# Performance work log

Hardware: AMD Instinct MI355X
Metric: run time of the kernel (lower is better)

Reference implementation:

```python
import jax, jax.numpy as jnp
import numpy as np

D_MODEL = 256
D_INNER = 512      # expand=2 * d_model
D_STATE = 16
D_CONV = 4
DT_RANK = 16       # ceil(d_model/16)
BT, N = 16, 1024


def setup_inputs() -> dict:
    key = jax.random.key(0)
    ks = jax.random.split(key, 8)
    def w(k, shape, scale=0.02):
        return jax.random.normal(k, shape, dtype=jnp.float32) * scale
    token = jax.random.normal(ks[0], (BT, N, D_MODEL), dtype=jnp.float32)
    in_proj_w = w(ks[1], (2 * D_INNER, D_MODEL))
    conv_w = w(ks[2], (D_INNER, D_CONV), 0.1)          # depthwise conv taps
    conv_b = jnp.zeros((D_INNER,), jnp.float32)
    x_proj_w = w(ks[3], (DT_RANK + 2 * D_STATE, D_INNER))
    dt_proj_w = w(ks[4], (D_INNER, DT_RANK), 0.1)
    # softplus^{-1}(0.01): standard Mamba dt bias init scale
    dt_proj_b = jnp.log(jnp.expm1(jnp.full((D_INNER,), 0.01, jnp.float32)))
    # S4D-real init: A_log = log(1..d_state) per channel
    A_log = jnp.log(jnp.tile(jnp.arange(1, D_STATE + 1, dtype=jnp.float32), (D_INNER, 1)))
    D_skip = jnp.ones((D_INNER,), jnp.float32)
    out_proj_w = w(ks[5], (D_MODEL, D_INNER))
    return dict(token=token, in_proj_w=in_proj_w, conv_w=conv_w, conv_b=conv_b,
                x_proj_w=x_proj_w, dt_proj_w=dt_proj_w, dt_proj_b=dt_proj_b,
                A_log=A_log, D_skip=D_skip, out_proj_w=out_proj_w)


def _mamba_fwd(token, in_proj_w, conv_w, conv_b, x_proj_w, dt_proj_w, dt_proj_b,
               A_log, D_skip, out_proj_w):
    B, L, _ = token.shape
    # input projection -> gate z and conv branch x
    xz = jnp.einsum('blc,ec->ble', token, in_proj_w)        # (B,L,2*Di)
    x, z = jnp.split(xz, 2, axis=-1)                        # (B,L,Di) each
    # depthwise causal conv1d, kernel D_CONV, left padding D_CONV-1
    xp = jnp.pad(x, ((0, 0), (D_CONV - 1, 0), (0, 0)))
    x_conv = conv_b + sum(xp[:, k:k + L, :] * conv_w[:, k] for k in range(D_CONV))
    x = jax.nn.silu(x_conv)
    # data-dependent dt, B, C
    dbc = jnp.einsum('bld,ed->ble', x, x_proj_w)            # (B,L,dt_rank+2*Ns)
    dt, Bm, Cm = jnp.split(dbc, [DT_RANK, DT_RANK + D_STATE], axis=-1)
    delta = jax.nn.softplus(jnp.einsum('blr,dr->bld', dt, dt_proj_w) + dt_proj_b)
    A = -jnp.exp(A_log)                                     # (Di,Ns), all negative
    dA = jnp.exp(delta[..., None] * A)                      # (B,L,Di,Ns)
    dBu = delta[..., None] * Bm[:, :, None, :] * x[..., None]  # (B,L,Di,Ns)
    # selective scan over sequence: h_t = dA_t * h_{t-1} + dBu_t ; y_t = <h_t, C_t>
    def step(h, inp):
        dA_t, dBu_t, C_t = inp                              # (B,Di,Ns),(B,Di,Ns),(B,Ns)
        h = dA_t * h + dBu_t
        y = jnp.einsum('bdn,bn->bd', h, C_t)
        return h, y
    h0 = jnp.zeros((B, D_INNER, D_STATE), token.dtype)
    xs = (dA.transpose(1, 0, 2, 3), dBu.transpose(1, 0, 2, 3), Cm.transpose(1, 0, 2))
    _, ys = jax.lax.scan(step, h0, xs)                      # (L,B,Di)
    y = ys.transpose(1, 0, 2) + x * D_skip
    y = y * jax.nn.silu(z)
    return jnp.einsum('bld,cd->blc', y, out_proj_w)         # (B,L,d_model)


def reference(token, in_proj_w, conv_w, conv_b, x_proj_w, dt_proj_w, dt_proj_b,
              A_log, D_skip, out_proj_w):
    return _mamba_fwd(token, in_proj_w, conv_w, conv_b, x_proj_w, dt_proj_w,
                      dt_proj_b, A_log, D_skip, out_proj_w)
```

## Files before the change

kernel.cpp:

```cpp
#include <hip/hip_runtime.h>
#include <cstddef>

static constexpr int kDModel = 256;
static constexpr int kDInner = 512;
static constexpr int kDState = 16;
static constexpr int kDtRank = 16;
static constexpr int kB = 16;
static constexpr int kL = 1024;
static constexpr int kTok = kB * kL;
static constexpr int kDbcW = kDtRank + 2 * kDState;
static constexpr int kT = 64;
static constexpr int kG = kL / kT;

typedef __attribute__((ext_vector_type(8))) short short8;
typedef __attribute__((ext_vector_type(4))) float f32x4;

__device__ __forceinline__ float siluf(float x) {
  return x / (1.0f + __expf(-x));
}

__device__ __forceinline__ void split2(float a, float b, unsigned& h, unsigned& l) {
  const unsigned ua = __float_as_uint(a), ub = __float_as_uint(b);
  const unsigned ha = ua & 0xffff0000u, hb = ub & 0xffff0000u;
  h = (ha >> 16) | hb;
  const float la = a - __uint_as_float(ha);
  const float lb = b - __uint_as_float(hb);
  l = (__float_as_uint(la) >> 16) | (__float_as_uint(lb) & 0xffff0000u);
}

__global__ __launch_bounds__(256) void split_k(
    const float* __restrict__ src, unsigned short* __restrict__ H,
    unsigned short* __restrict__ L, int n4)
{
  const int i = (int)(blockIdx.x * 256 + threadIdx.x);
  if (i >= n4) return;
  const float4 v = ((const float4*)src)[i];
  unsigned h0, l0, h1, l1;
  split2(v.x, v.y, h0, l0);
  split2(v.z, v.w, h1, l1);
  ((uint2*)H)[i] = make_uint2(h0, h1);
  ((uint2*)L)[i] = make_uint2(l0, l1);
}

__device__ __forceinline__ void gload16(const unsigned short* g, unsigned short* l) {
  __builtin_amdgcn_global_load_lds(
      (const __attribute__((address_space(1))) unsigned int*)g,
      (__attribute__((address_space(3))) unsigned int*)l, 16, 0, 0);
}

template <int EPI>
__global__ __launch_bounds__(256) void gemm_bt_mfma(
    const unsigned short* __restrict__ Ahg, const unsigned short* __restrict__ Alg, int lda,
    const unsigned short* __restrict__ Bhg, const unsigned short* __restrict__ Blg, int ldb,
    float* __restrict__ C, int ldc, int K,
    float* __restrict__ out2)
{
  __shared__ __align__(16) unsigned short lds[12288];
  unsigned short* Ah = lds;
  unsigned short* Al = lds + 4096;
  unsigned short* Bh = lds + 8192;
  unsigned short* Bl = lds + 10240;

  const int tid = (int)threadIdx.x;
  const int m0 = blockIdx.x * 128;
  const int n0 = blockIdx.y * 64;
  const int lane = tid & 63;
  const int w = tid >> 6, wm = w >> 1, wn = w & 1;
  const int fr = lane & 15;
  const int j = lane >> 4;

  const int srow = lane >> 2;
  const int sslot = lane & 3;

  f32x4 acc[4][2];
#pragma unroll
  for (int i = 0; i < 4; ++i)
#pragma unroll
    for (int jj = 0; jj < 2; ++jj) acc[i][jj] = (f32x4){0.f, 0.f, 0.f, 0.f};

  const int r1 = 16 * w + srow;
  const int r2 = r1 + 64;
  const int s1 = (sslot ^ ((r1 >> 1) & 3)) * 8;
  const int s2 = (sslot ^ ((r2 >> 1) & 3)) * 8;
  const unsigned short* A1h = Ahg + (size_t)(m0 + r1) * lda + s1;
  const unsigned short* A2h = Ahg + (size_t)(m0 + r2) * lda + s2;
  const unsigned short* A1l = Alg + (size_t)(m0 + r1) * lda + s1;
  const unsigned short* A2l = Alg + (size_t)(m0 + r2) * lda + s2;
  const unsigned short* B1h = Bhg + (size_t)(n0 + r1) * ldb + s1;
  const unsigned short* B1l = Blg + (size_t)(n0 + r1) * ldb + s1;
  unsigned short* dA1 = Ah + 512 * w;
  unsigned short* dA2 = Ah + 512 * (w + 4);
  unsigned short* dL1 = Al + 512 * w;
  unsigned short* dL2 = Al + 512 * (w + 4);
  unsigned short* dB1 = Bh + 512 * w;
  unsigned short* dB2 = Bl + 512 * w;

  for (int k0 = 0; k0 < K; k0 += 32) {
    __syncthreads();
    gload16(A1h + k0, dA1);
    gload16(A2h + k0, dA2);
    gload16(A1l + k0, dL1);
    gload16(A2l + k0, dL2);
    gload16(B1h + k0, dB1);
    gload16(B1l + k0, dB2);
    __syncthreads();

    short8 ah[4], al[4], bh[2], bl[2];
#pragma unroll
    for (int mi = 0; mi < 4; ++mi) {
      const int R = wm * 64 + mi * 16 + fr;
      const int off = R * 32 + ((j ^ ((R >> 1) & 3)) * 8);
      ah[mi] = *(const short8*)&Ah[off];
      al[mi] = *(const short8*)&Al[off];
    }
#pragma unroll
    for (int ni = 0; ni < 2; ++ni) {
      const int R = wn * 32 + ni * 16 + fr;
      const int off = R * 32 + ((j ^ ((R >> 1) & 3)) * 8);
      bh[ni] = *(const short8*)&Bh[off];
      bl[ni] = *(const short8*)&Bl[off];
    }
#pragma unroll
    for (int mi = 0; mi < 4; ++mi)
#pragma unroll
      for (int ni = 0; ni < 2; ++ni) {
        acc[mi][ni] = __builtin_amdgcn_mfma_f32_16x16x32_bf16(ah[mi], bh[ni], acc[mi][ni], 0, 0, 0);
        acc[mi][ni] = __builtin_amdgcn_mfma_f32_16x16x32_bf16(ah[mi], bl[ni], acc[mi][ni], 0, 0, 0);
        acc[mi][ni] = __builtin_amdgcn_mfma_f32_16x16x32_bf16(al[mi], bh[ni], acc[mi][ni], 0, 0, 0);
      }
  }

  float* Cb;
  int nbase, ldout;
  if (EPI == 1) {
    Cb = (n0 < kDInner) ? C : out2;
    nbase = (n0 & (kDInner - 1)) + wn * 32 + fr;
    ldout = kDInner;
  } else {
    Cb = C;
    nbase = n0 + wn * 32 + fr;
    ldout = ldc;
  }
#pragma unroll
  for (int mi = 0; mi < 4; ++mi) {
    const int mrow = m0 + wm * 64 + mi * 16 + (lane >> 4) * 4;
#pragma unroll
    for (int ni = 0; ni < 2; ++ni)
#pragma unroll
      for (int r = 0; r < 4; ++r)
        Cb[(size_t)(mrow + r) * ldout + nbase + ni * 16] = acc[mi][ni][r];
  }
}

template <int EPI>
__global__ __launch_bounds__(256) void gemm_bt_f32(
    const float* __restrict__ A, int lda,
    const float* __restrict__ B, int ldb,
    float* __restrict__ C, int ldc,
    int N, int K,
    float* __restrict__ out2,
    const float* __restrict__ bias)
{
  constexpr int BM = 64, BN = 64, BK = 16;
  __shared__ float As[BK][BM];
  __shared__ float Bs[BK][BN];
  const int m0 = blockIdx.x * BM;
  const int n0 = blockIdx.y * BN;
  const int tid = (int)threadIdx.x;
  const int tx = tid & 15;
  const int ty = tid >> 4;
  const int lr = tid >> 2;
  const int lk = (tid & 3) * 4;

  float acc[4][4] = {};

  for (int k0 = 0; k0 < K; k0 += BK) {
    const float4 a4 = *(const float4*)(A + (size_t)(m0 + lr) * lda + k0 + lk);
    float4 b4 = make_float4(0.f, 0.f, 0.f, 0.f);
    if (n0 + lr < N)
      b4 = *(const float4*)(B + (size_t)(n0 + lr) * ldb + k0 + lk);
    __syncthreads();
    As[lk + 0][lr] = a4.x; As[lk + 1][lr] = a4.y;
    As[lk + 2][lr] = a4.z; As[lk + 3][lr] = a4.w;
    Bs[lk + 0][lr] = b4.x; Bs[lk + 1][lr] = b4.y;
    Bs[lk + 2][lr] = b4.z; Bs[lk + 3][lr] = b4.w;
    __syncthreads();
#pragma unroll
    for (int kk = 0; kk < BK; ++kk) {
      const float4 av = *(const float4*)&As[kk][ty * 4];
      const float4 bv = *(const float4*)&Bs[kk][tx * 4];
      const float a[4] = {av.x, av.y, av.z, av.w};
      const float b[4] = {bv.x, bv.y, bv.z, bv.w};
#pragma unroll
      for (int i = 0; i < 4; ++i)
#pragma unroll
        for (int j = 0; j < 4; ++j)
          acc[i][j] = fmaf(a[i], b[j], acc[i][j]);
    }
  }

#pragma unroll
  for (int i = 0; i < 4; ++i) {
    const int m = m0 + ty * 4 + i;
#pragma unroll
    for (int j = 0; j < 4; ++j) {
      const int n = n0 + tx * 4 + j;
      float v = acc[i][j];
      if (EPI == 0) {
        if (n < N) C[(size_t)m * ldc + n] = v;
      } else {
        v += bias[n];
        v = fmaxf(v, 0.f) + __logf(1.f + __expf(-fabsf(v)));
        if (n < N) C[(size_t)m * ldc + n] = v;
      }
    }
  }
}

__global__ __launch_bounds__(256) void conv_silu_k(
    const float* __restrict__ x, const float* __restrict__ cw,
    const float* __restrict__ cb, float* __restrict__ xc)
{
  const int id = (int)(blockIdx.x * 256 + threadIdx.x);
  const int dq = (id & 127) * 4;
  const int t  = id >> 7;
  const int l  = t & (kL - 1);

  float w[4][4];
#pragma unroll
  for (int j = 0; j < 4; ++j) {
    const float4 wt = *(const float4*)(cw + (size_t)(dq + j) * 4);
    w[j][0] = wt.x; w[j][1] = wt.y; w[j][2] = wt.z; w[j][3] = wt.w;
  }
  float r[4] = {cb[dq + 0], cb[dq + 1], cb[dq + 2], cb[dq + 3]};
#pragma unroll
  for (int k = 0; k < 4; ++k) {
    const int ll = l + k - 3;
    if (ll >= 0) {
      const float4 xv = *(const float4*)(x + (size_t)(t + k - 3) * kDInner + dq);
      r[0] = fmaf(xv.x, w[0][k], r[0]);
      r[1] = fmaf(xv.y, w[1][k], r[1]);
      r[2] = fmaf(xv.z, w[2][k], r[2]);
      r[3] = fmaf(xv.w, w[3][k], r[3]);
    }
  }
  *(float4*)(xc + (size_t)t * kDInner + dq) =
      make_float4(siluf(r[0]), siluf(r[1]), siluf(r[2]), siluf(r[3]));
}

__global__ __launch_bounds__(256) void scan_part1(
    const float* __restrict__ delta, const float* __restrict__ xc,
    const float* __restrict__ dbc,  const float* __restrict__ A_log,
    float* __restrict__ Pbuf, float* __restrict__ hloc)
{
  const int tid = (int)(blockIdx.x * 256 + threadIdx.x);
  const int lane = tid & 63;
  const int gw = __builtin_amdgcn_readfirstlane(tid >> 6);
  const int dg = gw & 7;
  const int c  = (gw >> 3) & (kG - 1);
  const int b  = gw >> 7;
  const int d  = dg * 64 + lane;
  const int t0 = b * kL + c * kT;

  float A2[kDState], h[kDState];
#pragma unroll
  for (int n = 0; n < kDState; ++n) {
    A2[n] = -__expf(A_log[d * kDState + n]) * 1.44269504088896f;
    h[n] = 0.f;
  }
  const float* dp = delta + (size_t)t0 * kDInner + d;
  const float* xp = xc + (size_t)t0 * kDInner + d;
  float sd = 0.f;
#pragma unroll 2
  for (int l = 0; l < kT; ++l) {
    const float dl = dp[(size_t)l * kDInner];
    const float xv = xp[(size_t)l * kDInner];
    const float* bp = dbc + (size_t)(t0 + l) * kDbcW + kDtRank;
    const float s = dl * xv;
    sd += dl;
#pragma unroll
    for (int n = 0; n < kDState; ++n) {
      const float dA = __builtin_amdgcn_exp2f(dl * A2[n]);
      h[n] = fmaf(dA, h[n], s * bp[n]);
    }
  }
  const size_t o0 = (size_t)((b * kG + c) * kDState) * kDInner + d;
#pragma unroll
  for (int n = 0; n < kDState; ++n) {
    Pbuf[o0 + (size_t)n * kDInner] = __builtin_amdgcn_exp2f(A2[n] * sd);
    hloc[o0 + (size_t)n * kDInner] = h[n];
  }
}

__global__ __launch_bounds__(256) void scan_part2(
    const float* __restrict__ Pbuf, const float* __restrict__ hloc,
    float* __restrict__ hin)
{
  const int t = (int)(blockIdx.x * 256 + threadIdx.x);
  const int d = t & (kDInner - 1);
  const int n = (t >> 9) & (kDState - 1);
  const int b = t >> 13;
  float carry = 0.f;
#pragma unroll
  for (int c = 0; c < kG; ++c) {
    const size_t idx = (size_t)((b * kG + c) * kDState + n) * kDInner + d;
    hin[idx] = carry;
    carry = fmaf(Pbuf[idx], carry, hloc[idx]);
  }
}

__global__ __launch_bounds__(256) void scan_part3(
    const float* __restrict__ delta, const float* __restrict__ xc,
    const float* __restrict__ dbc,  const float* __restrict__ z,
    const float* __restrict__ A_log, const float* __restrict__ D_skip,
    const float* __restrict__ hin,
    unsigned short* __restrict__ yh, unsigned short* __restrict__ yl)
{
  const int tid = (int)(blockIdx.x * 256 + threadIdx.x);
  const int lane = tid & 63;
  const int gw = __builtin_amdgcn_readfirstlane(tid >> 6);
  const int dg = gw & 7;
  const int c  = (gw >> 3) & (kG - 1);
  const int b  = gw >> 7;
  const int d  = dg * 64 + lane;
  const int t0 = b * kL + c * kT;

  const size_t o0 = (size_t)((b * kG + c) * kDState) * kDInner + d;
  float A2[kDState], h[kDState];
#pragma unroll
  for (int n = 0; n < kDState; ++n) {
    A2[n] = -__expf(A_log[d * kDState + n]) * 1.44269504088896f;
    h[n] = hin[o0 + (size_t)n * kDInner];
  }
  const float Dv = D_skip[d];
  const float* dp = delta + (size_t)t0 * kDInner + d;
  const float* xp = xc + (size_t)t0 * kDInner + d;
  const float* zp = z + (size_t)t0 * kDInner + d;
  unsigned short* yhp = yh + (size_t)t0 * kDInner + d;
  unsigned short* ylp = yl + (size_t)t0 * kDInner + d;
#pragma unroll 2
  for (int l = 0; l < kT; ++l) {
    const float dl = dp[(size_t)l * kDInner];
    const float xv = xp[(size_t)l * kDInner];
    const float zv = zp[(size_t)l * kDInner];
    const float* bp = dbc + (size_t)(t0 + l) * kDbcW + kDtRank;
    const float s = dl * xv;
    float yv = 0.f;
#pragma unroll
    for (int n = 0; n < kDState; ++n) {
      const float dA = __builtin_amdgcn_exp2f(dl * A2[n]);
      h[n] = fmaf(dA, h[n], s * bp[n]);
      yv = fmaf(h[n], bp[kDState + n], yv);
    }
    yv = fmaf(xv, Dv, yv);
    yv *= zv / (1.f + __expf(-zv));
    const unsigned u = __float_as_uint(yv);
    const unsigned hi = u & 0xffff0000u;
    yhp[(size_t)l * kDInner] = (unsigned short)(u >> 16);
    ylp[(size_t)l * kDInner] =
        (unsigned short)(__float_as_uint(yv - __uint_as_float(hi)) >> 16);
  }
}

extern "C" void kernel_launch(void* const* d_in, const int* in_sizes, int n_in,
                              void* d_out, int out_size, void* d_ws, size_t ws_size,
                              hipStream_t stream) {
  (void)in_sizes; (void)n_in; (void)out_size; (void)ws_size;
  const float* token     = (const float*)d_in[0];
  const float* in_proj_w = (const float*)d_in[1];
  const float* conv_w    = (const float*)d_in[2];
  const float* conv_b    = (const float*)d_in[3];
  const float* x_proj_w  = (const float*)d_in[4];
  const float* dt_proj_w = (const float*)d_in[5];
  const float* dt_proj_b = (const float*)d_in[6];
  const float* A_log     = (const float*)d_in[7];
  const float* D_skip    = (const float*)d_in[8];
  const float* out_proj_w= (const float*)d_in[9];
  float* out = (float*)d_out;

  float* ws = (float*)d_ws;
  float* xbuf  = ws;
  float* zbuf  = xbuf + (size_t)kTok * kDInner;
  float* xcbuf = zbuf + (size_t)kTok * kDInner;
  float* dbc   = xcbuf + (size_t)kTok * kDInner;
  float* ybuf  = dbc + (size_t)kTok * kDbcW;
  float* hin   = ybuf + (size_t)kTok * kDInner;
  float* delta = xbuf;

  unsigned short* tokH = (unsigned short*)ybuf;
  unsigned short* tokL = tokH + (size_t)kTok * kDModel;
  float* Pbuf = ybuf;
  float* hloc = ybuf + (size_t)kB * kG * kDState * kDInner;
  unsigned short* yh = (unsigned short*)ybuf;
  unsigned short* yl = yh + (size_t)kTok * kDInner;
  unsigned short* ipH = (unsigned short*)hin;
  unsigned short* ipL = ipH + (size_t)2 * kDInner * kDModel;
  unsigned short* opH = (unsigned short*)(hin + (size_t)kB * kDInner * kG * kDState);
  unsigned short* opL = opH + (size_t)kDModel * kDInner;

  split_k<<<(kTok * kDModel / 4) / 256, 256, 0, stream>>>(token, tokH, tokL,
                                                          kTok * kDModel / 4);
  split_k<<<(2 * kDInner * kDModel / 4) / 256, 256, 0, stream>>>(
      in_proj_w, ipH, ipL, 2 * kDInner * kDModel / 4);
  split_k<<<(kDModel * kDInner / 4) / 256, 256, 0, stream>>>(
      out_proj_w, opH, opL, kDModel * kDInner / 4);

  {
    dim3 g(kTok / 128, (2 * kDInner) / 64);
    gemm_bt_mfma<1><<<g, 256, 0, stream>>>(tokH, tokL, kDModel, ipH, ipL, kDModel,
                                           xbuf, kDInner, kDModel, zbuf);
  }
  conv_silu_k<<<(kTok * (kDInner / 4)) / 256, 256, 0, stream>>>(xbuf, conv_w, conv_b, xcbuf);
  {
    dim3 g(kTok / 64, 1);
    gemm_bt_f32<0><<<g, 256, 0, stream>>>(xcbuf, kDInner, x_proj_w, kDInner,
                                          dbc, kDbcW, kDbcW, kDInner,
                                          nullptr, nullptr);
  }
  {
    dim3 g(kTok / 64, kDInner / 64);
    gemm_bt_f32<2><<<g, 256, 0, stream>>>(dbc, kDbcW, dt_proj_w, kDtRank,
                                          delta, kDInner, kDInner, kDtRank,
                                          nullptr, dt_proj_b);
  }
  scan_part1<<<(kB * kG * 8) / 4, 256, 0, stream>>>(delta, xcbuf, dbc, A_log,
                                                    Pbuf, hloc);
  scan_part2<<<(kB * kDInner * kDState) / 256, 256, 0, stream>>>(Pbuf, hloc, hin);
  scan_part3<<<(kB * kG * 8) / 4, 256, 0, stream>>>(delta, xcbuf, dbc, zbuf,
                                                    A_log, D_skip, hin, yh, yl);
  {
    dim3 g(kTok / 128, kDModel / 64);
    gemm_bt_mfma<0><<<g, 256, 0, stream>>>(yh, yl, kDInner, opH, opL, kDInner,
                                           out, kDModel, kDInner, nullptr);
  }
}
```

Measured before the change: 282.4 us.

## Fuse dt projection into scan kernels and double-buffer MFMA GEMM LDS loads

Removes the separate dt_proj GEMM+softplus kernel. Both scan passes now recompute delta per token and channel from the dbc row using per-thread dt_proj weights, which saves writing and reading the 32 MB delta buffer twice. The MFMA GEMM also gets a two-stage LDS double buffer, so the next K tile's global-to-LDS loads are issued before computing on the current one, with explicit vmcnt waits. The trade-off is extra FMAs and transcendentals recomputed in both scan passes, plus double the LDS footprint, which may reduce occupancy.

```diff
diff --git a/kernel.cpp b/kernel.cpp
--- a/kernel.cpp
+++ b/kernel.cpp
@@ -55,11 +55,7 @@
     float* __restrict__ C, int ldc, int K,
     float* __restrict__ out2)
 {
-  __shared__ __align__(16) unsigned short lds[12288];
-  unsigned short* Ah = lds;
-  unsigned short* Al = lds + 4096;
-  unsigned short* Bh = lds + 8192;
-  unsigned short* Bl = lds + 10240;
+  __shared__ __align__(16) unsigned short lds[24576];
 
   const int tid = (int)threadIdx.x;
   const int m0 = blockIdx.x * 128;
@@ -88,37 +84,44 @@
   const unsigned short* A2l = Alg + (size_t)(m0 + r2) * lda + s2;
   const unsigned short* B1h = Bhg + (size_t)(n0 + r1) * ldb + s1;
   const unsigned short* B1l = Blg + (size_t)(n0 + r1) * ldb + s1;
-  unsigned short* dA1 = Ah + 512 * w;
-  unsigned short* dA2 = Ah + 512 * (w + 4);
-  unsigned short* dL1 = Al + 512 * w;
-  unsigned short* dL2 = Al + 512 * (w + 4);
-  unsigned short* dB1 = Bh + 512 * w;
-  unsigned short* dB2 = Bl + 512 * w;
-
-  for (int k0 = 0; k0 < K; k0 += 32) {
-    __syncthreads();
-    gload16(A1h + k0, dA1);
-    gload16(A2h + k0, dA2);
-    gload16(A1l + k0, dL1);
-    gload16(A2l + k0, dL2);
-    gload16(B1h + k0, dB1);
-    gload16(B1l + k0, dB2);
-    __syncthreads();
+
+  auto STAGE = [&](unsigned short* buf, int k0) {
+    gload16(A1h + k0, buf + 512 * w);
+    gload16(A2h + k0, buf + 512 * (w + 4));
+    gload16(A1l + k0, buf + 4096 + 512 * w);
+    gload16(A2l + k0, buf + 4096 + 512 * (w + 4));
+    gload16(B1h + k0, buf + 8192 + 512 * w);
+    gload16(B1l + k0, buf + 10240 + 512 * w);
+  };
+
+  const int nt = K >> 5;
+  unsigned short* cur = lds;
+  unsigned short* nxt = lds + 12288;
+
+  STAGE(cur, 0);
+  for (int it = 0; it < nt; ++it) {
+    if (it + 1 < nt) {
+      STAGE(nxt, (it + 1) << 5);
+      asm volatile("s_waitcnt vmcnt(6)" ::: "memory");
+    } else {
+      asm volatile("s_waitcnt vmcnt(0)" ::: "memory");
+    }
+    __builtin_amdgcn_s_barrier();
 
     short8 ah[4], al[4], bh[2], bl[2];
 #pragma unroll
     for (int mi = 0; mi < 4; ++mi) {
       const int R = wm * 64 + mi * 16 + fr;
       const int off = R * 32 + ((j ^ ((R >> 1) & 3)) * 8);
-      ah[mi] = *(const short8*)&Ah[off];
-      al[mi] = *(const short8*)&Al[off];
+      ah[mi] = *(const short8*)&cur[off];
+      al[mi] = *(const short8*)&cur[4096 + off];
     }
 #pragma unroll
     for (int ni = 0; ni < 2; ++ni) {
       const int R = wn * 32 + ni * 16 + fr;
       const int off = R * 32 + ((j ^ ((R >> 1) & 3)) * 8);
-      bh[ni] = *(const short8*)&Bh[off];
-      bl[ni] = *(const short8*)&Bl[off];
+      bh[ni] = *(const short8*)&cur[8192 + off];
+      bl[ni] = *(const short8*)&cur[10240 + off];
     }
 #pragma unroll
     for (int mi = 0; mi < 4; ++mi)
@@ -128,6 +131,8 @@
         acc[mi][ni] = __builtin_amdgcn_mfma_f32_16x16x32_bf16(ah[mi], bl[ni], acc[mi][ni], 0, 0, 0);
         acc[mi][ni] = __builtin_amdgcn_mfma_f32_16x16x32_bf16(al[mi], bh[ni], acc[mi][ni], 0, 0, 0);
       }
+    __builtin_amdgcn_s_barrier();
+    unsigned short* t = cur; cur = nxt; nxt = t;
   }
 
   float* Cb;
@@ -152,14 +157,11 @@
   }
 }
 
-template <int EPI>
 __global__ __launch_bounds__(256) void gemm_bt_f32(
     const float* __restrict__ A, int lda,
     const float* __restrict__ B, int ldb,
     float* __restrict__ C, int ldc,
-    int N, int K,
-    float* __restrict__ out2,
-    const float* __restrict__ bias)
+    int N, int K)
 {
   constexpr int BM = 64, BN = 64, BK = 16;
   __shared__ float As[BK][BM];
@@ -205,14 +207,7 @@
 #pragma unroll
     for (int j = 0; j < 4; ++j) {
       const int n = n0 + tx * 4 + j;
-      float v = acc[i][j];
-      if (EPI == 0) {
-        if (n < N) C[(size_t)m * ldc + n] = v;
-      } else {
-        v += bias[n];
-        v = fmaxf(v, 0.f) + __logf(1.f + __expf(-fabsf(v)));
-        if (n < N) C[(size_t)m * ldc + n] = v;
-      }
+      if (n < N) C[(size_t)m * ldc + n] = acc[i][j];
     }
   }
 }
@@ -248,9 +243,18 @@
       make_float4(siluf(r[0]), siluf(r[1]), siluf(r[2]), siluf(r[3]));
 }
 
+__device__ __forceinline__ float delta_of(const float* __restrict__ row,
+                                          const float* __restrict__ W, float bias) {
+  float a = bias;
+#pragma unroll
+  for (int r = 0; r < kDtRank; ++r) a = fmaf(row[r], W[r], a);
+  return fmaxf(a, 0.f) + __logf(1.f + __expf(-fabsf(a)));
+}
+
 __global__ __launch_bounds__(256) void scan_part1(
-    const float* __restrict__ delta, const float* __restrict__ xc,
-    const float* __restrict__ dbc,  const float* __restrict__ A_log,
+    const float* __restrict__ xc, const float* __restrict__ dbc,
+    const float* __restrict__ A_log,
+    const float* __restrict__ dtW, const float* __restrict__ dtB,
     float* __restrict__ Pbuf, float* __restrict__ hloc)
 {
   const int tid = (int)(blockIdx.x * 256 + threadIdx.x);
@@ -262,26 +266,29 @@
   const int d  = dg * 64 + lane;
   const int t0 = b * kL + c * kT;
 
-  float A2[kDState], h[kDState];
+  float A2[kDState], h[kDState], W[kDtRank];
 #pragma unroll
   for (int n = 0; n < kDState; ++n) {
     A2[n] = -__expf(A_log[d * kDState + n]) * 1.44269504088896f;
     h[n] = 0.f;
   }
-  const float* dp = delta + (size_t)t0 * kDInner + d;
+#pragma unroll
+  for (int r = 0; r < kDtRank; ++r) W[r] = dtW[d * kDtRank + r];
+  const float bias = dtB[d];
+
   const float* xp = xc + (size_t)t0 * kDInner + d;
   float sd = 0.f;
 #pragma unroll 2
   for (int l = 0; l < kT; ++l) {
-    const float dl = dp[(size_t)l * kDInner];
     const float xv = xp[(size_t)l * kDInner];
-    const float* bp = dbc + (size_t)(t0 + l) * kDbcW + kDtRank;
+    const float* row = dbc + (size_t)(t0 + l) * kDbcW;
+    const float dl = delta_of(row, W, bias);
     const float s = dl * xv;
     sd += dl;
 #pragma unroll
     for (int n = 0; n < kDState; ++n) {
       const float dA = __builtin_amdgcn_exp2f(dl * A2[n]);
-      h[n] = fmaf(dA, h[n], s * bp[n]);
+      h[n] = fmaf(dA, h[n], s * row[kDtRank + n]);
     }
   }
   const size_t o0 = (size_t)((b * kG + c) * kDState) * kDInner + d;
@@ -310,9 +317,10 @@
 }
 
 __global__ __launch_bounds__(256) void scan_part3(
-    const float* __restrict__ delta, const float* __restrict__ xc,
-    const float* __restrict__ dbc,  const float* __restrict__ z,
-    const float* __restrict__ A_log, const float* __restrict__ D_skip,
+    const float* __restrict__ xc, const float* __restrict__ dbc,
+    const float* __restrict__ z,  const float* __restrict__ A_log,
+    const float* __restrict__ D_skip,
+    const float* __restrict__ dtW, const float* __restrict__ dtB,
     const float* __restrict__ hin,
     unsigned short* __restrict__ yh, unsigned short* __restrict__ yl)
 {
@@ -326,31 +334,34 @@
   const int t0 = b * kL + c * kT;
 
   const size_t o0 = (size_t)((b * kG + c) * kDState) * kDInner + d;
-  float A2[kDState], h[kDState];
+  float A2[kDState], h[kDState], W[kDtRank];
 #pragma unroll
   for (int n = 0; n < kDState; ++n) {
     A2[n] = -__expf(A_log[d * kDState + n]) * 1.44269504088896f;
     h[n] = hin[o0 + (size_t)n * kDInner];
   }
+#pragma unroll
+  for (int r = 0; r < kDtRank; ++r) W[r] = dtW[d * kDtRank + r];
+  const float bias = dtB[d];
   const float Dv = D_skip[d];
-  const float* dp = delta + (size_t)t0 * kDInner + d;
+
   const float* xp = xc + (size_t)t0 * kDInner + d;
   const float* zp = z + (size_t)t0 * kDInner + d;
   unsigned short* yhp = yh + (size_t)t0 * kDInner + d;
   unsigned short* ylp = yl + (size_t)t0 * kDInner + d;
 #pragma unroll 2
   for (int l = 0; l < kT; ++l) {
-    const float dl = dp[(size_t)l * kDInner];
     const float xv = xp[(size_t)l * kDInner];
     const float zv = zp[(size_t)l * kDInner];
-    const float* bp = dbc + (size_t)(t0 + l) * kDbcW + kDtRank;
+    const float* row = dbc + (size_t)(t0 + l) * kDbcW;
+    const float dl = delta_of(row, W, bias);
     const float s = dl * xv;
     float yv = 0.f;
 #pragma unroll
     for (int n = 0; n < kDState; ++n) {
       const float dA = __builtin_amdgcn_exp2f(dl * A2[n]);
-      h[n] = fmaf(dA, h[n], s * bp[n]);
-      yv = fmaf(h[n], bp[kDState + n], yv);
+      h[n] = fmaf(dA, h[n], s * row[kDtRank + n]);
+      yv = fmaf(h[n], row[kDtRank + kDState + n], yv);
     }
     yv = fmaf(xv, Dv, yv);
     yv *= zv / (1.f + __expf(-zv));
@@ -385,7 +396,6 @@
   float* dbc   = xcbuf + (size_t)kTok * kDInner;
   float* ybuf  = dbc + (size_t)kTok * kDbcW;
   float* hin   = ybuf + (size_t)kTok * kDInner;
-  float* delta = xbuf;
 
   unsigned short* tokH = (unsigned short*)ybuf;
   unsigned short* tokL = tokH + (size_t)kTok * kDModel;
@@ -413,21 +423,16 @@
   conv_silu_k<<<(kTok * (kDInner / 4)) / 256, 256, 0, stream>>>(xbuf, conv_w, conv_b, xcbuf);
   {
     dim3 g(kTok / 64, 1);
-    gemm_bt_f32<0><<<g, 256, 0, stream>>>(xcbuf, kDInner, x_proj_w, kDInner,
-                                          dbc, kDbcW, kDbcW, kDInner,
-                                          nullptr, nullptr);
-  }
-  {
-    dim3 g(kTok / 64, kDInner / 64);
-    gemm_bt_f32<2><<<g, 256, 0, stream>>>(dbc, kDbcW, dt_proj_w, kDtRank,
-                                          delta, kDInner, kDInner, kDtRank,
-                                          nullptr, dt_proj_b);
-  }
-  scan_part1<<<(kB * kG * 8) / 4, 256, 0, stream>>>(delta, xcbuf, dbc, A_log,
+    gemm_bt_f32<<<g, 256, 0, stream>>>(xcbuf, kDInner, x_proj_w, kDInner,
+                                       dbc, kDbcW, kDbcW, kDInner);
+  }
+  scan_part1<<<(kB * kG * 8) / 4, 256, 0, stream>>>(xcbuf, dbc, A_log,
+                                                    dt_proj_w, dt_proj_b,
                                                     Pbuf, hloc);
   scan_part2<<<(kB * kDInner * kDState) / 256, 256, 0, stream>>>(Pbuf, hloc, hin);
-  scan_part3<<<(kB * kG * 8) / 4, 256, 0, stream>>>(delta, xcbuf, dbc, zbuf,
-                                                    A_log, D_skip, hin, yh, yl);
+  scan_part3<<<(kB * kG * 8) / 4, 256, 0, stream>>>(xcbuf, dbc, zbuf, A_log,
+                                                    D_skip, dt_proj_w, dt_proj_b,
+                                                    hin, yh, yl);
   {
     dim3 g(kTok / 128, kDModel / 64);
     gemm_bt_mfma<0><<<g, 256, 0, stream>>>(yh, yl, kDInner, opH, opL, kDInner,
```

New measurement: 283.6 us. No clear change (+0.4%).
